# Performance work log

Hardware: AMD Instinct MI355X
Metric: run time of the kernel (lower is better)

## Reference

```python
import jax, jax.numpy as jnp
import numpy as np

B, N, D_MODEL, H, DH, D_INNER = 4, 1024, 512, 8, 64, 2048
SQRTD = float(np.sqrt(DH))


def _ln(x, g, b, eps=1e-5):
    mu = jnp.mean(x, axis=-1, keepdims=True)
    var = jnp.var(x, axis=-1, keepdims=True)
    return (x - mu) * jax.lax.rsqrt(var + eps) * g + b


def setup_inputs() -> dict:
    key = jax.random.key(0)
    ks = jax.random.split(key, 8)
    s = 1.0 / np.sqrt(D_MODEL)
    si = 1.0 / np.sqrt(D_INNER)
    return {
        "Z": jax.random.normal(ks[0], (B, N, D_MODEL), jnp.float32),
        "D": jax.random.uniform(ks[1], (B, N, N), jnp.float32),
        "new_mask": jnp.zeros((B, N, N), jnp.float32),
        "mask": jnp.ones((B, N, N), jnp.float32),
        "Wqkv": jax.random.uniform(ks[2], (3 * D_MODEL, D_MODEL), jnp.float32, -s, s),
        "bqkv": jnp.zeros((3 * D_MODEL,), jnp.float32),
        "Wo": jax.random.uniform(ks[3], (D_MODEL, H * DH), jnp.float32, -s, s),
        "g1": jnp.ones((D_MODEL,), jnp.float32),
        "b1": jnp.zeros((D_MODEL,), jnp.float32),
        "g2": jnp.ones((D_MODEL,), jnp.float32),
        "b2": jnp.zeros((D_MODEL,), jnp.float32),
        "Wp1": jax.random.uniform(ks[4], (D_INNER, D_MODEL), jnp.float32, -s, s),
        "bp1": jnp.zeros((D_INNER,), jnp.float32),
        "Wp2": jax.random.uniform(ks[5], (D_MODEL, D_INNER), jnp.float32, -si, si),
        "bp2": jnp.zeros((D_MODEL,), jnp.float32),
        "gamma": jnp.ones((1,), jnp.float32),
    }


def reference(Z, D, new_mask, mask, Wqkv, bqkv, Wo, g1, b1, g2, b2, Wp1, bp1, Wp2, bp2, gamma):
    inp = Z
    Zn = _ln(Z, g1, b1)
    qkv = (Zn @ Wqkv.T + bqkv).reshape(B, N, H, 3 * DH)
    # chunk order in torch: Z2=value, Z3=query, Z4=key
    v = qkv[..., :DH]
    q = qkv[..., DH:2 * DH]
    k = qkv[..., 2 * DH:]
    # scores: [b, h, n, m]
    W = jnp.einsum('bnhd,bmhd->bhnm', q, k) / SQRTD
    W = W + new_mask[:, None] - (gamma * D)[:, None]
    W = jax.nn.softmax(W, axis=3) * mask[:, None]
    attn = jnp.einsum('bhnm,bmhd->bnhd', W, v).reshape(B, N, D_MODEL)
    attn_out = jax.nn.leaky_relu(attn) @ Wo.T
    Z2 = attn_out + inp
    Zn2 = _ln(Z2, g2, b2)
    return jax.nn.relu(Zn2 @ Wp1.T + bp1) @ Wp2.T + bp2 + Z2
```

## Files before the change

### kernel.cpp

```cpp
#include <hip/hip_runtime.h>
#include <hip/hip_bf16.h>
#include <cstddef>
#include <cstdint>

#define Bv 4
#define Nv 1024
#define DM 512
#define Hh 8
#define DHv 64
#define TOKc 4096

typedef __attribute__((ext_vector_type(4))) float f32x4;
typedef __attribute__((ext_vector_type(8))) short s16x8;

__device__ __forceinline__ uint32_t f2bf_bits(float f) {
    uint32_t x = __float_as_uint(f);
    return (x + 0x7FFFu + ((x >> 16) & 1u)) >> 16;
}
__device__ __forceinline__ short f2bf(float f) { return (short)f2bf_bits(f); }
__device__ __forceinline__ float bf2f(short s) {
    return __uint_as_float(((uint32_t)(uint16_t)s) << 16);
}

__device__ __forceinline__ void g2lds16(const void* g, void* l) {
    __builtin_amdgcn_global_load_lds(
        (const __attribute__((address_space(1))) void*)g,
        (__attribute__((address_space(3))) void*)l, 16, 0, 0);
}

__global__ __launch_bounds__(256) void prep_conv(
    const float* __restrict__ Dm, const float* __restrict__ nm,
    const float* __restrict__ mk, const float* __restrict__ gamma,
    uint32_t* __restrict__ Bm,
    const float* __restrict__ W0, const float* __restrict__ W1,
    const float* __restrict__ W2, const float* __restrict__ W3,
    short* __restrict__ D0, short* __restrict__ D1,
    short* __restrict__ D2, short* __restrict__ D3)
{
    int bid = blockIdx.x;
    if (bid < 4096) {
        int o = (bid * 256 + threadIdx.x) * 4;
        float g = gamma[0];
        size_t row = o >> 10;
        int p = o & 1023;
        int t = p >> 5;
        const float* Dr = Dm + row * 1024 + t * 32;
        const float* Nr = nm + row * 1024 + t * 32;
        const float* Mr = mk + row * 1024 + t * 32;
        uint4 ov;
        uint32_t* po = &ov.x;
#pragma unroll
        for (int q = 0; q < 4; q++) {
            int pp = (p & 31) + q;
            int j = (pp >> 1) & 15, half = pp & 1;
            int key = half * 16 + j;
            float bias = Nr[key] - g * Dr[key];
            po[q] = f2bf_bits(bias) | (f2bf_bits(Mr[key]) << 16);
        }
        *(uint4*)&Bm[o] = ov;
    } else {
        int cid = bid - 4096;
        const float* s; short* d; int base;
        if (cid < 768)       { s = W0; d = D0; base = cid * 1024; }
        else if (cid < 1024) { s = W1; d = D1; base = (cid - 768) * 1024; }
        else if (cid < 2048) { s = W2; d = D2; base = (cid - 1024) * 1024; }
        else                 { s = W3; d = D3; base = (cid - 2048) * 1024; }
        int i = base + threadIdx.x * 4;
        float4 v = *(const float4*)&s[i];
        short4 o = { f2bf(v.x), f2bf(v.y), f2bf(v.z), f2bf(v.w) };
        *(short4*)&d[i] = o;
    }
}

__global__ __launch_bounds__(256) void ln_kernel(
    const float* __restrict__ X, const float* __restrict__ g,
    const float* __restrict__ bb, short* __restrict__ Y)
{
    __shared__ float red[8];
    int row = blockIdx.x, tid = threadIdx.x;
    const float* x = X + (size_t)row * DM;
    float v0 = x[tid], v1 = x[tid + 256];
    float s = v0 + v1, ss = v0 * v0 + v1 * v1;
#pragma unroll
    for (int o = 32; o > 0; o >>= 1) {
        s += __shfl_xor(s, o);
        ss += __shfl_xor(ss, o);
    }
    int lane = tid & 63, wid = tid >> 6;
    if (lane == 0) { red[wid] = s; red[4 + wid] = ss; }
    __syncthreads();
    float S = red[0] + red[1] + red[2] + red[3];
    float SS = red[4] + red[5] + red[6] + red[7];
    float mean = S * (1.f / DM);
    float var = SS * (1.f / DM) - mean * mean;
    float rstd = rsqrtf(var + 1e-5f);
    short* y = Y + (size_t)row * DM;
    y[tid]       = f2bf((v0 - mean) * rstd * g[tid]       + bb[tid]);
    y[tid + 256] = f2bf((v1 - mean) * rstd * g[tid + 256] + bb[tid + 256]);
}

template <int EPI, int BM, int BN>
__global__ __launch_bounds__(256) void gemm_bf16(
    const short* __restrict__ A, const short* __restrict__ Bw,
    const float* __restrict__ bias, const float* __restrict__ resid,
    void* __restrict__ C0, short* __restrict__ C2, short* __restrict__ C3,
    int M, int N, int Ks, int Kst)
{
    constexpr int FI = BM / 32, FJ = BN / 32;
    __shared__ short As0[BM * 32];
    __shared__ short As1[BM * 32];
    __shared__ short Bs0[BN * 32];
    __shared__ short Bs1[BN * 32];
    int tid = threadIdx.x;
    int lane = tid & 63, wave = tid >> 6;
    int bm = blockIdx.y * BM, bn = blockIdx.x * BN;
    int wm = (wave >> 1) * (BM / 2), wn = (wave & 1) * (BN / 2);
    int n_lo = lane & 15, quad = lane >> 4;

    f32x4 acc[FI][FJ] = {};

    int koff = (EPI == 4) ? blockIdx.z * Ks : 0;
    int lrow = lane >> 2, lchunk = (lane & 3) * 8;
    const short* Ag = A + (size_t)(bm + wave * (BM / 4) + lrow) * Kst + koff + lchunk;
    const short* Bg = Bw + (size_t)(bn + wave * (BN / 4) + lrow) * Kst + koff + lchunk;

    for (int k0 = 0; k0 < Ks; k0 += 64) {
        __syncthreads();
#pragma unroll
        for (int r = 0; r < BM / 64; r++) {
            g2lds16(Ag + (size_t)r * 16 * Kst + k0,      &As0[(wave * (BM / 4) + r * 16) * 32]);
            g2lds16(Ag + (size_t)r * 16 * Kst + k0 + 32, &As1[(wave * (BM / 4) + r * 16) * 32]);
        }
#pragma unroll
        for (int r = 0; r < BN / 64; r++) {
            g2lds16(Bg + (size_t)r * 16 * Kst + k0,      &Bs0[(wave * (BN / 4) + r * 16) * 32]);
            g2lds16(Bg + (size_t)r * 16 * Kst + k0 + 32, &Bs1[(wave * (BN / 4) + r * 16) * 32]);
        }
        __syncthreads();
        s16x8 af0[FI], af1[FI], bf0[FJ], bf1[FJ];
#pragma unroll
        for (int i = 0; i < FI; i++) {
            af0[i] = *(const s16x8*)&As0[(wm + i * 16 + n_lo) * 32 + quad * 8];
            af1[i] = *(const s16x8*)&As1[(wm + i * 16 + n_lo) * 32 + quad * 8];
        }
#pragma unroll
        for (int j = 0; j < FJ; j++) {
            bf0[j] = *(const s16x8*)&Bs0[(wn + j * 16 + n_lo) * 32 + quad * 8];
            bf1[j] = *(const s16x8*)&Bs1[(wn + j * 16 + n_lo) * 32 + quad * 8];
        }
#pragma unroll
        for (int i = 0; i < FI; i++)
#pragma unroll
            for (int j = 0; j < FJ; j++)
                acc[i][j] = __builtin_amdgcn_mfma_f32_16x16x32_bf16(
                    af0[i], bf0[j], acc[i][j], 0, 0, 0);
#pragma unroll
        for (int i = 0; i < FI; i++)
#pragma unroll
            for (int j = 0; j < FJ; j++)
                acc[i][j] = __builtin_amdgcn_mfma_f32_16x16x32_bf16(
                    af1[i], bf1[j], acc[i][j], 0, 0, 0);
    }

#pragma unroll
    for (int i = 0; i < FI; i++) {
#pragma unroll
        for (int j = 0; j < FJ; j++) {
            int col = bn + wn + j * 16 + n_lo;
#pragma unroll
            for (int r = 0; r < 4; r++) {
                int m = bm + wm + i * 16 + quad * 4 + r;
                float v = acc[i][j][r];
                if (EPI == 0) {
                    v += bias[col];
                    int hh = col / 192;
                    int rr = col - hh * 192;
                    int part = rr >> 6, dd = rr & 63;
                    int bI = m >> 10, nI = m & 1023;
                    if (part == 0)
                        ((short*)C0)[((size_t)((bI * Hh + hh) * DHv + dd)) * Nv + nI] = f2bf(v);
                    else if (part == 1)
                        C2[((size_t)((bI * Hh + hh) * Nv + nI)) * DHv + dd] = f2bf(v);
                    else
                        C3[((size_t)((bI * Hh + hh) * Nv + nI)) * DHv + dd] = f2bf(v);
                } else if (EPI == 1) {
                    ((float*)C0)[(size_t)m * N + col] = v + resid[(size_t)m * N + col];
                } else if (EPI == 2) {
                    v += bias[col];
                    ((short*)C0)[(size_t)m * N + col] = f2bf(v > 0.f ? v : 0.f);
                } else {
                    ((short*)C0)[(size_t)blockIdx.z * M * N + (size_t)m * N + col] = f2bf(v);
                }
            }
        }
    }
}

__global__ __launch_bounds__(256) void combine_mlp2(
    const short* __restrict__ P, const float* __restrict__ bias,
    const float* __restrict__ resid, float* __restrict__ out)
{
    int i = (blockIdx.x * 256 + threadIdx.x) * 4;
    float4 rz = *(const float4*)&resid[i];
    float4 bz = *(const float4*)&bias[i & 511];
    short4 p0 = *(const short4*)&P[i];
    short4 p1 = *(const short4*)&P[i + 2097152];
    short4 p2 = *(const short4*)&P[i + 2 * 2097152];
    short4 p3 = *(const short4*)&P[i + 3 * 2097152];
    float4 o;
    o.x = bf2f(p0.x) + bf2f(p1.x) + bf2f(p2.x) + bf2f(p3.x) + bz.x + rz.x;
    o.y = bf2f(p0.y) + bf2f(p1.y) + bf2f(p2.y) + bf2f(p3.y) + bz.y + rz.y;
    o.z = bf2f(p0.z) + bf2f(p1.z) + bf2f(p2.z) + bf2f(p3.z) + bz.z + rz.z;
    o.w = bf2f(p0.w) + bf2f(p1.w) + bf2f(p2.w) + bf2f(p3.w) + bz.w + rz.w;
    *(float4*)&out[i] = o;
}

__global__ __launch_bounds__(512) void attn_mfma(
    const short* __restrict__ Q, const short* __restrict__ K,
    const short* __restrict__ Vt, const uint32_t* __restrict__ Bm,
    short* __restrict__ attn_l)
{
    __shared__ short Ksh[64 * 64];
    __shared__ short Vsh[64 * 64];
    __shared__ uint32_t Bsh[128 * 64];
    __shared__ short Ph[8][16 * 72];

    int tid = threadIdx.x, lane = tid & 63, wave = tid >> 6;
    int n_lo = lane & 15, quad = lane >> 4;

    int bid = blockIdx.x;
    int x = bid & 7, inner = bid >> 3;
    int bh = x * 4 + (inner & 3);
    int qt = inner >> 2;
    int b = bh >> 3, h = bh & 7;
    int q0 = qt * 128;
    int qw = q0 + wave * 16;

    const short* Qp = Q + ((size_t)((b * Hh + h) * Nv + qw)) * DHv;
    const short* Kp = K + ((size_t)((b * Hh + h) * Nv)) * DHv;
    const short* Vp = Vt + ((size_t)((b * Hh + h) * DHv)) * Nv;
    const uint32_t* Bp = Bm + ((size_t)(b * Nv + q0)) * Nv;

    s16x8 a0 = *(const s16x8*)&Qp[n_lo * DHv + quad * 8];
    s16x8 a1 = *(const s16x8*)&Qp[n_lo * DHv + 32 + quad * 8];

    f32x4 O[4] = {};
    float lacc[4] = {0.f, 0.f, 0.f, 0.f};
    short* Pw = Ph[wave];

    for (int kt = 0; kt < 16; ++kt) {
        int key0 = kt * 64;
        __syncthreads();
        g2lds16(Kp + (size_t)(key0 + wave * 8 + (lane >> 3)) * DHv + (lane & 7) * 8,
                &Ksh[wave * 8 * 64]);
        g2lds16(Vp + (size_t)(wave * 8 + (lane >> 3)) * Nv + key0 + (lane & 7) * 8,
                &Vsh[wave * 8 * 64]);
#pragma unroll
        for (int s = 0; s < 4; s++) {
            int si = wave * 4 + s;
            g2lds16(Bp + (size_t)(si * 4 + (lane >> 4)) * Nv + key0 + (lane & 15) * 4,
                    &Bsh[si * 4 * 64]);
        }
        __syncthreads();

#pragma unroll
        for (int c = 0; c < 2; c++) {
            s16x8 k0a = *(const s16x8*)&Ksh[(c * 32 + n_lo) * 64 + quad * 8];
            s16x8 k0b = *(const s16x8*)&Ksh[(c * 32 + n_lo) * 64 + 32 + quad * 8];
            s16x8 k1a = *(const s16x8*)&Ksh[(c * 32 + 16 + n_lo) * 64 + quad * 8];
            s16x8 k1b = *(const s16x8*)&Ksh[(c * 32 + 16 + n_lo) * 64 + 32 + quad * 8];
            f32x4 z = {0.f, 0.f, 0.f, 0.f};
            f32x4 s0 = __builtin_amdgcn_mfma_f32_16x16x32_bf16(
                a1, k0b, __builtin_amdgcn_mfma_f32_16x16x32_bf16(a0, k0a, z, 0, 0, 0), 0, 0, 0);
            f32x4 s1 = __builtin_amdgcn_mfma_f32_16x16x32_bf16(
                a1, k1b, __builtin_amdgcn_mfma_f32_16x16x32_bf16(a0, k1a, z, 0, 0, 0), 0, 0, 0);
#pragma unroll
            for (int i = 0; i < 4; i++) {
                int row = quad * 4 + i;
                uint2 u = *(const uint2*)&Bsh[(wave * 16 + row) * 64 + c * 32 + n_lo * 2];
                float e0 = __expf(fminf(s0[i] * 0.125f + __uint_as_float(u.x << 16), 60.f));
                float e1 = __expf(fminf(s1[i] * 0.125f + __uint_as_float(u.y << 16), 60.f));
                lacc[i] += e0 + e1;
                Pw[row * 72 + c * 32 + n_lo]      = f2bf(e0 * __uint_as_float(u.x & 0xFFFF0000u));
                Pw[row * 72 + c * 32 + 16 + n_lo] = f2bf(e1 * __uint_as_float(u.y & 0xFFFF0000u));
            }
        }

#pragma unroll
        for (int c = 0; c < 2; c++) {
            s16x8 pa = *(const s16x8*)&Pw[n_lo * 72 + c * 32 + quad * 8];
#pragma unroll
            for (int t = 0; t < 4; t++) {
                s16x8 vb = *(const s16x8*)&Vsh[(t * 16 + n_lo) * 64 + c * 32 + quad * 8];
                O[t] = __builtin_amdgcn_mfma_f32_16x16x32_bf16(pa, vb, O[t], 0, 0, 0);
            }
        }
    }

#pragma unroll
    for (int i = 0; i < 4; i++)
#pragma unroll
        for (int off = 1; off < 16; off <<= 1) lacc[i] += __shfl_xor(lacc[i], off);

    float inv[4];
#pragma unroll
    for (int i = 0; i < 4; i++) inv[i] = 1.f / lacc[i];
#pragma unroll
    for (int t = 0; t < 4; t++)
#pragma unroll
        for (int i = 0; i < 4; i++) {
            float o = O[t][i] * inv[i];
            o = o > 0.f ? o : 0.01f * o;
            attn_l[((size_t)(b * Nv + qw + quad * 4 + i)) * DM + h * DHv + t * 16 + n_lo] = f2bf(o);
        }
}

extern "C" void kernel_launch(void* const* d_in, const int* in_sizes, int n_in,
                              void* d_out, int out_size, void* d_ws, size_t ws_size,
                              hipStream_t stream)
{
    const float* Z     = (const float*)d_in[0];
    const float* D     = (const float*)d_in[1];
    const float* nmsk  = (const float*)d_in[2];
    const float* msk   = (const float*)d_in[3];
    const float* Wqkv  = (const float*)d_in[4];
    const float* bqkv  = (const float*)d_in[5];
    const float* Wo    = (const float*)d_in[6];
    const float* g1    = (const float*)d_in[7];
    const float* b1    = (const float*)d_in[8];
    const float* g2    = (const float*)d_in[9];
    const float* b2    = (const float*)d_in[10];
    const float* Wp1   = (const float*)d_in[11];
    const float* bp1   = (const float*)d_in[12];
    const float* Wp2   = (const float*)d_in[13];
    const float* bp2   = (const float*)d_in[14];
    const float* gamma = (const float*)d_in[15];
    float* out = (float*)d_out;
    char* w = (char*)d_ws;

    const size_t MB = 1048576;
    short*    WqkvB = (short*)(w);
    short*    WoB   = (short*)(w + 1572864);
    short*    Wp1B  = (short*)(w + 2 * MB);
    short*    Wp2B  = (short*)(w + 4 * MB);
    float*    Z2    = (float*)(w + 6 * MB);
    uint32_t* Bm    = (uint32_t*)(w + 14 * MB);
    short*    Zn    = (short*)(w + 30 * MB);
    short*    Qb    = (short*)(w + 34 * MB);
    short*    Kb    = (short*)(w + 38 * MB);
    short*    VtB   = (short*)(w + 42 * MB);
    short*    AtnL  = (short*)(w + 30 * MB);
    short*    Zn2   = (short*)(w + 14 * MB);
    short*    Hb    = (short*)(w + 18 * MB);
    short*    Pp    = (short*)(w + 34 * MB);

    prep_conv<<<7168, 256, 0, stream>>>(D, nmsk, msk, gamma, Bm,
                                        Wqkv, Wo, Wp1, Wp2, WqkvB, WoB, Wp1B, Wp2B);
    ln_kernel<<<TOKc, 256, 0, stream>>>(Z, g1, b1, Zn);
    gemm_bf16<0, 128, 128><<<dim3(12, 32), 256, 0, stream>>>(
        Zn, WqkvB, bqkv, nullptr, VtB, Qb, Kb, TOKc, 1536, 512, 512);
    attn_mfma<<<dim3(256), 512, 0, stream>>>(Qb, Kb, VtB, Bm, AtnL);
    gemm_bf16<1, 64, 64><<<dim3(8, 64), 256, 0, stream>>>(
        AtnL, WoB, nullptr, Z, Z2, nullptr, nullptr, TOKc, 512, 512, 512);
    ln_kernel<<<TOKc, 256, 0, stream>>>(Z2, g2, b2, Zn2);
    gemm_bf16<2, 128, 128><<<dim3(16, 32), 256, 0, stream>>>(
        Zn2, Wp1B, bp1, nullptr, Hb, nullptr, nullptr, TOKc, 2048, 512, 512);
    gemm_bf16<4, 128, 128><<<dim3(4, 32, 4), 256, 0, stream>>>(
        Hb, Wp2B, nullptr, nullptr, Pp, nullptr, nullptr, TOKc, 512, 512, 2048);
    combine_mlp2<<<2048, 256, 0, stream>>>(Pp, bp2, Z2, out);
}
```

Before: 242.6 us.

## Fuse first LayerNorm into prep kernel, shrink attention and QKV GEMM tiles

Folds the first LayerNorm into the prep/conversion kernel as extra blocks, saving one launch. The attention kernel drops to 4 waves with 64-query tiles and twice as many blocks, and the QKV GEMM uses 128x64 tiles with double the grid. The aim is better occupancy and more blocks to fill the GPU's CUs, at the cost of reloading K/V/bias tiles for more query tiles. The Bm bias loads in attention appear to assume the same per-wave mapping, so correctness relies on the 4-wave split covering 64 rows.

```diff
diff --git a/kernel.cpp b/kernel.cpp
--- a/kernel.cpp
+++ b/kernel.cpp
@@ -28,14 +28,16 @@
         (__attribute__((address_space(3))) void*)l, 16, 0, 0);
 }
 
-__global__ __launch_bounds__(256) void prep_conv(
+__global__ __launch_bounds__(256) void prep_conv_ln(
     const float* __restrict__ Dm, const float* __restrict__ nm,
     const float* __restrict__ mk, const float* __restrict__ gamma,
     uint32_t* __restrict__ Bm,
     const float* __restrict__ W0, const float* __restrict__ W1,
     const float* __restrict__ W2, const float* __restrict__ W3,
     short* __restrict__ D0, short* __restrict__ D1,
-    short* __restrict__ D2, short* __restrict__ D3)
+    short* __restrict__ D2, short* __restrict__ D3,
+    const float* __restrict__ Z, const float* __restrict__ g1,
+    const float* __restrict__ b1, short* __restrict__ Zn)
 {
     int bid = blockIdx.x;
     if (bid < 4096) {
@@ -58,7 +60,7 @@
             po[q] = f2bf_bits(bias) | (f2bf_bits(Mr[key]) << 16);
         }
         *(uint4*)&Bm[o] = ov;
-    } else {
+    } else if (bid < 7168) {
         int cid = bid - 4096;
         const float* s; short* d; int base;
         if (cid < 768)       { s = W0; d = D0; base = cid * 1024; }
@@ -69,6 +71,28 @@
         float4 v = *(const float4*)&s[i];
         short4 o = { f2bf(v.x), f2bf(v.y), f2bf(v.z), f2bf(v.w) };
         *(short4*)&d[i] = o;
+    } else {
+        __shared__ float red[8];
+        int row = bid - 7168, tid = threadIdx.x;
+        const float* x = Z + (size_t)row * DM;
+        float v0 = x[tid], v1 = x[tid + 256];
+        float s = v0 + v1, ss = v0 * v0 + v1 * v1;
+#pragma unroll
+        for (int o = 32; o > 0; o >>= 1) {
+            s += __shfl_xor(s, o);
+            ss += __shfl_xor(ss, o);
+        }
+        int lane = tid & 63, wid = tid >> 6;
+        if (lane == 0) { red[wid] = s; red[4 + wid] = ss; }
+        __syncthreads();
+        float S = red[0] + red[1] + red[2] + red[3];
+        float SS = red[4] + red[5] + red[6] + red[7];
+        float mean = S * (1.f / DM);
+        float var = SS * (1.f / DM) - mean * mean;
+        float rstd = rsqrtf(var + 1e-5f);
+        short* y = Zn + (size_t)row * DM;
+        y[tid]       = f2bf((v0 - mean) * rstd * g1[tid]       + b1[tid]);
+        y[tid + 256] = f2bf((v1 - mean) * rstd * g1[tid + 256] + b1[tid + 256]);
     }
 }
 
@@ -215,15 +239,15 @@
     *(float4*)&out[i] = o;
 }
 
-__global__ __launch_bounds__(512) void attn_mfma(
+__global__ __launch_bounds__(256) void attn_mfma(
     const short* __restrict__ Q, const short* __restrict__ K,
     const short* __restrict__ Vt, const uint32_t* __restrict__ Bm,
     short* __restrict__ attn_l)
 {
     __shared__ short Ksh[64 * 64];
     __shared__ short Vsh[64 * 64];
-    __shared__ uint32_t Bsh[128 * 64];
-    __shared__ short Ph[8][16 * 72];
+    __shared__ uint32_t Bsh[64 * 64];
+    __shared__ short Ph[4][16 * 72];
 
     int tid = threadIdx.x, lane = tid & 63, wave = tid >> 6;
     int n_lo = lane & 15, quad = lane >> 4;
@@ -233,7 +257,7 @@
     int bh = x * 4 + (inner & 3);
     int qt = inner >> 2;
     int b = bh >> 3, h = bh & 7;
-    int q0 = qt * 128;
+    int q0 = qt * 64;
     int qw = q0 + wave * 16;
 
     const short* Qp = Q + ((size_t)((b * Hh + h) * Nv + qw)) * DHv;
@@ -251,10 +275,14 @@
     for (int kt = 0; kt < 16; ++kt) {
         int key0 = kt * 64;
         __syncthreads();
-        g2lds16(Kp + (size_t)(key0 + wave * 8 + (lane >> 3)) * DHv + (lane & 7) * 8,
-                &Ksh[wave * 8 * 64]);
-        g2lds16(Vp + (size_t)(wave * 8 + (lane >> 3)) * Nv + key0 + (lane & 7) * 8,
-                &Vsh[wave * 8 * 64]);
+#pragma unroll
+        for (int s = 0; s < 2; s++) {
+            int si = wave * 2 + s;
+            g2lds16(Kp + (size_t)(key0 + si * 8 + (lane >> 3)) * DHv + (lane & 7) * 8,
+                    &Ksh[si * 8 * 64]);
+            g2lds16(Vp + (size_t)(si * 8 + (lane >> 3)) * Nv + key0 + (lane & 7) * 8,
+                    &Vsh[si * 8 * 64]);
+        }
 #pragma unroll
         for (int s = 0; s < 4; s++) {
             int si = wave * 4 + s;
@@ -354,12 +382,13 @@
     short*    Hb    = (short*)(w + 18 * MB);
     short*    Pp    = (short*)(w + 34 * MB);
 
-    prep_conv<<<7168, 256, 0, stream>>>(D, nmsk, msk, gamma, Bm,
-                                        Wqkv, Wo, Wp1, Wp2, WqkvB, WoB, Wp1B, Wp2B);
-    ln_kernel<<<TOKc, 256, 0, stream>>>(Z, g1, b1, Zn);
-    gemm_bf16<0, 128, 128><<<dim3(12, 32), 256, 0, stream>>>(
+    prep_conv_ln<<<11264, 256, 0, stream>>>(D, nmsk, msk, gamma, Bm,
+                                            Wqkv, Wo, Wp1, Wp2,
+                                            WqkvB, WoB, Wp1B, Wp2B,
+                                            Z, g1, b1, Zn);
+    gemm_bf16<0, 128, 64><<<dim3(24, 32), 256, 0, stream>>>(
         Zn, WqkvB, bqkv, nullptr, VtB, Qb, Kb, TOKc, 1536, 512, 512);
-    attn_mfma<<<dim3(256), 512, 0, stream>>>(Qb, Kb, VtB, Bm, AtnL);
+    attn_mfma<<<dim3(512), 256, 0, stream>>>(Qb, Kb, VtB, Bm, AtnL);
     gemm_bf16<1, 64, 64><<<dim3(8, 64), 256, 0, stream>>>(
         AtnL, WoB, nullptr, Z, Z2, nullptr, nullptr, TOKc, 512, 512, 512);
     ln_kernel<<<TOKc, 256, 0, stream>>>(Z2, g2, b2, Zn2);
```

Result: faster. 230.7 us (-4.9%).
